# Kernel tuning notes

Measured on AMD Instinct MI355X. Metric: run time of the kernel, lower is better.

The kernel has to match this reference:

```python
import jax, jax.numpy as jnp
import numpy as np

E, H, BLOCK = 1024, 64, 2048

def setup_inputs() -> dict:
    key = jax.random.key(0)
    kx, kk, kq, kv = jax.random.split(key, 4)
    s = 1.0 / np.sqrt(E)
    return {
        "x": jax.random.normal(kx, (16, 2048, E), dtype=jnp.float32),
        "Wk": jax.random.uniform(kk, (E, H), jnp.float32, -s, s),
        "Wq": jax.random.uniform(kq, (E, H), jnp.float32, -s, s),
        "Wv": jax.random.uniform(kv, (E, H), jnp.float32, -s, s),
    }

def reference(x, Wk, Wq, Wv):
    B, T, C = x.shape
    k = x @ Wk  # [B,T,H]
    q = x @ Wq
    v = x @ Wv
    scale = jnp.asarray(H, x.dtype) ** -0.5
    wei = jnp.einsum("bth,bsh->bts", q, k) * scale  # [B,T,T]
    causal = jnp.tril(jnp.ones((T, T), dtype=bool))
    wei = jnp.where(causal, wei, -jnp.inf)
    wei = jax.nn.softmax(wei, axis=-1)
    # dropout is identity in eval mode
    return jnp.einsum("bts,bsh->bth", wei, v)
```

## Files before the change

kernel.cpp:

```cpp
#include <hip/hip_runtime.h>


typedef __bf16 bf16x8 __attribute__((ext_vector_type(8)));
typedef __bf16 bf16x4 __attribute__((ext_vector_type(4)));
typedef float f32x4 __attribute__((ext_vector_type(4)));

constexpr int kE = 1024;
constexpr int kH = 64;
constexpr int kT = 2048;
constexpr int kB = 16;
constexpr int kM = kB * kT;
constexpr float kQScale = 0.125f * 1.44269504088896340736f;

#define MFMA16(a, b, c) __builtin_amdgcn_mfma_f32_16x16x32_bf16((a), (b), (c), 0, 0, 0)

__device__ __forceinline__ void gl_lds16(const void* g, void* l) {
    __builtin_amdgcn_global_load_lds(
        (const __attribute__((address_space(1))) void*)g,
        (__attribute__((address_space(3))) void*)l, 16, 0, 0);
}

__global__ __launch_bounds__(256)
void prep_w(const float* __restrict__ Wq, const float* __restrict__ Wk,
            const float* __restrict__ Wv, __bf16* __restrict__ WbT)
{
    __shared__ float tl[64][65];
    const int mat = blockIdx.x >> 4;
    const int k0 = (blockIdx.x & 15) * 64;
    const float* src = (mat == 0) ? Wq : (mat == 1) ? Wk : Wv;

    const int t = threadIdx.x;
    const int kr = t >> 2;
    const int cg = (t & 3) * 16;
    #pragma unroll
    for (int i = 0; i < 4; ++i) {
        float4 v = *(const float4*)&src[(size_t)(k0 + kr) * kH + cg + 4 * i];
        tl[cg + 4 * i + 0][kr] = v.x;
        tl[cg + 4 * i + 1][kr] = v.y;
        tl[cg + 4 * i + 2][kr] = v.z;
        tl[cg + 4 * i + 3][kr] = v.w;
    }
    __syncthreads();
    const int nl = t >> 2;
    const int kg = (t & 3) * 16;
    bf16x8 o0, o1;
    #pragma unroll
    for (int j = 0; j < 8; ++j) {
        o0[j] = (__bf16)tl[nl][kg + j];
        o1[j] = (__bf16)tl[nl][kg + 8 + j];
    }
    *(bf16x8*)&WbT[(size_t)(mat * 64 + nl) * kE + k0 + kg] = o0;
    *(bf16x8*)&WbT[(size_t)(mat * 64 + nl) * kE + k0 + kg + 8] = o1;
}

__global__ __launch_bounds__(256)
void qkv(const float* __restrict__ x, const __bf16* __restrict__ WbT,
         __bf16* __restrict__ qo, __bf16* __restrict__ ko, __bf16* __restrict__ vT)
{
    __shared__ __align__(16) char Ab[2][16384];
    __shared__ __align__(16) char Bb[2][24576];

    const int t = threadIdx.x;
    const int lane = t & 63;
    const int w = t >> 6;
    const int l15 = lane & 15;
    const int Q = lane >> 4;
    const int row0 = blockIdx.x * 64;

    f32x4 acc[4][3];
    #pragma unroll
    for (int mt = 0; mt < 4; ++mt)
        #pragma unroll
        for (int nt = 0; nt < 3; ++nt) acc[mt][nt] = (f32x4){0.f, 0.f, 0.f, 0.f};

    auto stage = [&](int p, int k0) {
        #pragma unroll
        for (int i = 0; i < 4; ++i) {
            const int row = (w * 4 + i) * 4 + (lane >> 4);
            const int g = (lane & 15) ^ (i * 4 + (lane >> 4));
            gl_lds16(&x[(size_t)(row0 + row) * kE + k0 + g * 4],
                     &Ab[p][(w * 4 + i) * 1024]);
        }
        #pragma unroll
        for (int i = 0; i < 6; ++i) {
            const int n = (w * 6 + i) * 8 + (lane >> 3);
            const int g = (lane & 7) ^ (lane >> 3);
            gl_lds16(&WbT[(size_t)n * kE + k0 + g * 8],
                     &Bb[p][(w * 6 + i) * 1024]);
        }
    };

    stage(0, 0);
    __syncthreads();

    for (int c = 0; c < 16; ++c) {
        const int p = c & 1;
        if (c < 15) stage(1 - p, (c + 1) * 64);

        #pragma unroll
        for (int ks = 0; ks < 2; ++ks) {
            bf16x8 a4[4];
            #pragma unroll
            for (int mt = 0; mt < 4; ++mt) {
                const int row = mt * 16 + l15;
                float4 u0 = *(const float4*)&Ab[p][row * 256 + ((ks * 8 + Q * 2 + 0) ^ l15) * 16];
                float4 u1 = *(const float4*)&Ab[p][row * 256 + ((ks * 8 + Q * 2 + 1) ^ l15) * 16];
                bf16x8 a;
                a[0] = (__bf16)u0.x; a[1] = (__bf16)u0.y;
                a[2] = (__bf16)u0.z; a[3] = (__bf16)u0.w;
                a[4] = (__bf16)u1.x; a[5] = (__bf16)u1.y;
                a[6] = (__bf16)u1.z; a[7] = (__bf16)u1.w;
                a4[mt] = a;
            }
            #pragma unroll
            for (int nt = 0; nt < 3; ++nt) {
                const int n = w * 48 + nt * 16 + l15;
                bf16x8 b = *(const bf16x8*)&Bb[p][n * 128 + (((ks * 4 + Q) ^ (l15 & 7)) * 16)];
                #pragma unroll
                for (int mt = 0; mt < 4; ++mt)
                    acc[mt][nt] = MFMA16(a4[mt], b, acc[mt][nt]);
            }
        }
        __syncthreads();
    }

    const int batch = row0 >> 11;
    const int tr0 = row0 & 2047;
    #pragma unroll
    for (int nt = 0; nt < 3; ++nt) {
        const int col0 = w * 48 + nt * 16;
        const int mat = col0 >> 6;
        const int c = (col0 & 63) + l15;
        if (mat == 2) {
            #pragma unroll
            for (int mt = 0; mt < 4; ++mt) {
                const int trow = tr0 + mt * 16 + Q * 4;
                bf16x4 pk;
                #pragma unroll
                for (int r = 0; r < 4; ++r) pk[r] = (__bf16)acc[mt][nt][r];
                *(bf16x4*)&vT[((size_t)batch * kH + c) * kT + trow] = pk;
            }
        } else {
            __bf16* dst = (mat == 0) ? qo : ko;
            const float sc_ = (mat == 0) ? kQScale : 1.0f;
            #pragma unroll
            for (int mt = 0; mt < 4; ++mt)
                #pragma unroll
                for (int r = 0; r < 4; ++r) {
                    const size_t row = row0 + mt * 16 + Q * 4 + r;
                    dst[row * kH + c] = (__bf16)(acc[mt][nt][r] * sc_);
                }
        }
    }
}

__global__ __launch_bounds__(256, 2)
void attn(const __bf16* __restrict__ qm, const __bf16* __restrict__ km,
          const __bf16* __restrict__ vT, float* __restrict__ out)
{
    __shared__ __align__(16) char Kb[2][8192];
    __shared__ __align__(16) char Vb[2][8192];
    __shared__ __align__(16) __bf16 Ps[4][16][72];

    const int tid = threadIdx.x;
    const int lane = tid & 63;
    const int w = tid >> 6;
    const int l15 = lane & 15;
    const int Q = lane >> 4;

    const int xcd  = blockIdx.x & 7;
    const int slot = blockIdx.x >> 3;
    const int batch = xcd + ((slot & 1) << 3);
    const int tt = (slot & 1) ? (31 - (slot >> 1)) : (slot >> 1);
    const int q16 = tt * 4 + w;
    const int qrow = q16 * 16 + l15;
    const int last = tt;

    const __bf16* qb = qm + (size_t)batch * kT * kH;
    const __bf16* kb = km + (size_t)batch * kT * kH;
    const __bf16* vb = vT + (size_t)batch * kH * kT;

    auto stage = [&](int p, int s0) {
        #pragma unroll
        for (int i = 0; i < 2; ++i) {
            const int r = w * 16 + i * 8 + (lane >> 3);
            const int g = (lane & 7) ^ (lane >> 3);
            gl_lds16(&kb[(size_t)(s0 + r) * kH + g * 8],
                     &Kb[p][(w * 2 + i) * 1024]);
            gl_lds16(&vb[(size_t)r * kT + s0 + g * 8],
                     &Vb[p][(w * 2 + i) * 1024]);
        }
    };

    bf16x8 aq[2];
    aq[0] = *(const bf16x8*)&qb[(size_t)qrow * kH + Q * 8];
    aq[1] = *(const bf16x8*)&qb[(size_t)qrow * kH + 32 + Q * 8];

    f32x4 O[4];
    #pragma unroll
    for (int i = 0; i < 4; ++i) O[i] = (f32x4){0.f, 0.f, 0.f, 0.f};
    float m_ = -3.0e38f, l_ = 0.f;

    stage(0, 0);
    __syncthreads();

    for (int kt = 0; kt <= last; ++kt) {
        const int p = kt & 1;

        bf16x8 kf[8], vf[8];
        #pragma unroll
        for (int ks = 0; ks < 2; ++ks)
            #pragma unroll
            for (int nt = 0; nt < 4; ++nt)
                kf[ks * 4 + nt] = *(const bf16x8*)
                    &Kb[p][(nt * 16 + l15) * 128 + (((ks * 4 + Q) ^ (l15 & 7)) * 16)];
        #pragma unroll
        for (int ht = 0; ht < 4; ++ht)
            #pragma unroll
            for (int ss = 0; ss < 2; ++ss)
                vf[ht * 2 + ss] = *(const bf16x8*)
                    &Vb[p][(ht * 16 + l15) * 128 + (((ss * 4 + Q) ^ (l15 & 7)) * 16)];
        asm volatile("s_waitcnt lgkmcnt(0)" ::: "memory");

        if (kt < last) stage(1 - p, (kt + 1) * 64);

        f32x4 sacc[4];
        #pragma unroll
        for (int nt = 0; nt < 4; ++nt) sacc[nt] = (f32x4){0.f, 0.f, 0.f, 0.f};
        #pragma unroll
        for (int ks = 0; ks < 2; ++ks)
            #pragma unroll
            for (int nt = 0; nt < 4; ++nt)
                sacc[nt] = MFMA16(kf[ks * 4 + nt], aq[ks], sacc[nt]);

        if (kt == last) {
            const int s0 = kt * 64;
            #pragma unroll
            for (int nt = 0; nt < 4; ++nt)
                #pragma unroll
                for (int r = 0; r < 4; ++r)
                    if (s0 + nt * 16 + Q * 4 + r > qrow) sacc[nt][r] = -3.0e38f;
        }

        float mx = sacc[0][0];
        #pragma unroll
        for (int nt = 0; nt < 4; ++nt)
            #pragma unroll
            for (int r = 0; r < 4; ++r) mx = fmaxf(mx, sacc[nt][r]);
        mx = fmaxf(mx, __shfl_xor(mx, 16));
        mx = fmaxf(mx, __shfl_xor(mx, 32));
        const float mnew = fmaxf(m_, mx);
        const float alpha = __builtin_amdgcn_exp2f(m_ - mnew);
        float rs = 0.f;
        #pragma unroll
        for (int nt = 0; nt < 4; ++nt)
            #pragma unroll
            for (int r = 0; r < 4; ++r) {
                const float pv = __builtin_amdgcn_exp2f(sacc[nt][r] - mnew);
                sacc[nt][r] = pv;
                rs += pv;
            }
        rs += __shfl_xor(rs, 16);
        rs += __shfl_xor(rs, 32);
        l_ = l_ * alpha + rs;
        m_ = mnew;
        #pragma unroll
        for (int ht = 0; ht < 4; ++ht) O[ht] *= alpha;

        #pragma unroll
        for (int nt = 0; nt < 4; ++nt) {
            bf16x4 pk;
            #pragma unroll
            for (int r = 0; r < 4; ++r) pk[r] = (__bf16)sacc[nt][r];
            *(bf16x4*)&Ps[w][l15][nt * 16 + Q * 4] = pk;
        }
        bf16x8 pb0 = *(const bf16x8*)&Ps[w][l15][Q * 8];
        bf16x8 pb1 = *(const bf16x8*)&Ps[w][l15][32 + Q * 8];

        #pragma unroll
        for (int ht = 0; ht < 4; ++ht) {
            O[ht] = MFMA16(vf[ht * 2 + 0], pb0, O[ht]);
            O[ht] = MFMA16(vf[ht * 2 + 1], pb1, O[ht]);
        }

        __syncthreads();
    }

    const float inv = 1.0f / l_;
    float* orow = out + ((size_t)batch * kT + qrow) * kH;
    #pragma unroll
    for (int ht = 0; ht < 4; ++ht) {
        float4 o4;
        o4.x = O[ht][0] * inv; o4.y = O[ht][1] * inv;
        o4.z = O[ht][2] * inv; o4.w = O[ht][3] * inv;
        *(float4*)&orow[ht * 16 + Q * 4] = o4;
    }
}

extern "C" void kernel_launch(void* const* d_in, const int* in_sizes, int n_in,
                              void* d_out, int out_size, void* d_ws, size_t ws_size,
                              hipStream_t stream)
{
    (void)in_sizes; (void)n_in; (void)out_size; (void)ws_size;
    const float* x  = (const float*)d_in[0];
    const float* Wk = (const float*)d_in[1];
    const float* Wq = (const float*)d_in[2];
    const float* Wv = (const float*)d_in[3];

    __bf16* WbT  = (__bf16*)d_ws;
    __bf16* qb   = WbT + (size_t)192 * kE;
    __bf16* kbuf = qb + (size_t)kM * kH;
    __bf16* vT   = kbuf + (size_t)kM * kH;

    prep_w<<<48, 256, 0, stream>>>(Wq, Wk, Wv, WbT);
    qkv<<<kM / 64, 256, 0, stream>>>(x, WbT, qb, kbuf, vT);
    attn<<<512, 256, 0, stream>>>(qb, kbuf, vT, (float*)d_out);
}
```

Measured before the change: 242.1 us.

## Convert x to bf16 once in registers before staging into LDS

The A tile of x is now loaded from global memory into registers, converted to bf16 once, and written to LDS as bf16 after the MFMA loop. Previously the fp32 tile went straight to LDS through direct-to-LDS loads, and every wave converted it again on each read. The change halves LDS use and read traffic for A and removes the repeated conversions. In exchange the loads go through VGPRs, which raises register pressure, and the LDS write adds work before the barrier.

```diff
diff --git a/kernel.cpp b/kernel.cpp
--- a/kernel.cpp
+++ b/kernel.cpp
@@ -57,7 +57,7 @@
 void qkv(const float* __restrict__ x, const __bf16* __restrict__ WbT,
          __bf16* __restrict__ qo, __bf16* __restrict__ ko, __bf16* __restrict__ vT)
 {
-    __shared__ __align__(16) char Ab[2][16384];
+    __shared__ __align__(16) char Ab[2][8192];
     __shared__ __align__(16) char Bb[2][24576];
 
     const int t = threadIdx.x;
@@ -73,14 +73,7 @@
         #pragma unroll
         for (int nt = 0; nt < 3; ++nt) acc[mt][nt] = (f32x4){0.f, 0.f, 0.f, 0.f};
 
-    auto stage = [&](int p, int k0) {
-        #pragma unroll
-        for (int i = 0; i < 4; ++i) {
-            const int row = (w * 4 + i) * 4 + (lane >> 4);
-            const int g = (lane & 15) ^ (i * 4 + (lane >> 4));
-            gl_lds16(&x[(size_t)(row0 + row) * kE + k0 + g * 4],
-                     &Ab[p][(w * 4 + i) * 1024]);
-        }
+    auto stageB = [&](int p, int k0) {
         #pragma unroll
         for (int i = 0; i < 6; ++i) {
             const int n = (w * 6 + i) * 8 + (lane >> 3);
@@ -90,12 +83,36 @@
         }
     };
 
-    stage(0, 0);
+    float4 ar[4];
+    auto loadA = [&](int k0) {
+        #pragma unroll
+        for (int j = 0; j < 4; ++j) {
+            const int row = w * 16 + j * 4 + (lane >> 4);
+            ar[j] = *(const float4*)&x[(size_t)(row0 + row) * kE + k0 + l15 * 4];
+        }
+    };
+    auto writeA = [&](int p) {
+        #pragma unroll
+        for (int j = 0; j < 4; ++j) {
+            const int r = w * 16 + j * 4 + (lane >> 4);
+            bf16x4 pk;
+            pk[0] = (__bf16)ar[j].x; pk[1] = (__bf16)ar[j].y;
+            pk[2] = (__bf16)ar[j].z; pk[3] = (__bf16)ar[j].w;
+            *(bf16x4*)&Ab[p][r * 128 + (((l15 >> 1) ^ (r & 7)) * 16) + (l15 & 1) * 8] = pk;
+        }
+    };
+
+    loadA(0);
+    stageB(0, 0);
+    writeA(0);
     __syncthreads();
 
     for (int c = 0; c < 16; ++c) {
         const int p = c & 1;
-        if (c < 15) stage(1 - p, (c + 1) * 64);
+        if (c < 15) {
+            loadA((c + 1) * 64);
+            stageB(1 - p, (c + 1) * 64);
+        }
 
         #pragma unroll
         for (int ks = 0; ks < 2; ++ks) {
@@ -103,14 +120,8 @@
             #pragma unroll
             for (int mt = 0; mt < 4; ++mt) {
                 const int row = mt * 16 + l15;
-                float4 u0 = *(const float4*)&Ab[p][row * 256 + ((ks * 8 + Q * 2 + 0) ^ l15) * 16];
-                float4 u1 = *(const float4*)&Ab[p][row * 256 + ((ks * 8 + Q * 2 + 1) ^ l15) * 16];
-                bf16x8 a;
-                a[0] = (__bf16)u0.x; a[1] = (__bf16)u0.y;
-                a[2] = (__bf16)u0.z; a[3] = (__bf16)u0.w;
-                a[4] = (__bf16)u1.x; a[5] = (__bf16)u1.y;
-                a[6] = (__bf16)u1.z; a[7] = (__bf16)u1.w;
-                a4[mt] = a;
+                a4[mt] = *(const bf16x8*)
+                    &Ab[p][row * 128 + (((ks * 4 + Q) ^ (l15 & 7)) * 16)];
             }
             #pragma unroll
             for (int nt = 0; nt < 3; ++nt) {
@@ -121,6 +132,8 @@
                     acc[mt][nt] = MFMA16(a4[mt], b, acc[mt][nt]);
             }
         }
+
+        if (c < 15) writeA(1 - p);
         __syncthreads();
     }
 
```

Measured after the change: 243.8 us. No clear change (+0.7%).
